# Kernel optimization log

Hardware: AMD Instinct MI355X
Metric: run time of the kernel (lower is better)

Reference implementation:

```python
import jax, jax.numpy as jnp
import numpy as np

B, D_IN, N, K, L, D_OUT = 64, 1024, 50000, 32, 3, 256


def setup_inputs() -> dict:
    key = jax.random.key(0)
    k = jax.random.split(key, 7)
    x = jax.random.normal(k[0], (B, D_IN), dtype=jnp.float32)
    W0 = jax.random.normal(k[1], (N, D_IN), dtype=jnp.float32) * 0.02
    b0 = jax.random.normal(k[2], (N,), dtype=jnp.float32) * 0.02
    Wv = jax.random.normal(k[3], (L, N, K), dtype=jnp.float32) * 0.1
    Wout = jax.random.normal(k[4], (D_OUT, N), dtype=jnp.float32) * 0.02
    bout = jax.random.normal(k[5], (D_OUT,), dtype=jnp.float32) * 0.02
    src = jax.random.randint(k[6], (L, N, K), 0, N, dtype=jnp.int64)
    return {"x": x, "W0": W0, "b0": b0, "Wv": Wv, "Wout": Wout, "bout": bout, "src": src}


def reference(x, W0, b0, Wv, Wout, bout, src):
    # layer 0: dense input->sources, relu, transpose -> [N, B]
    h = jax.nn.relu(x @ W0.T + b0).T

    # each hidden layer: per-vertex gather of K source activations + 1xK matmul + relu
    def step(h_prev, layer):
        w, s = layer                      # w: [N, K], s: [N, K]
        gathered = h_prev[s]              # [N, K, B] irregular gather
        h_new = jax.nn.relu(jnp.einsum('nk,nkb->nb', w, gathered))
        return h_new, None

    h, _ = jax.lax.scan(step, h, (Wv, src))

    # last layer -> output Linear (the module's _linear_dummy)
    return h.T @ Wout.T + bout            # [B, D_OUT]
```

## Files before the change

kernel.cpp:

```cpp
#include <hip/hip_runtime.h>

#define NV 50000
#define NVP 50176
#define BDIM 64
#define DIN 1024
#define KFAN 32
#define DOUT 256
#define KSTEPS (DIN / 32)
#define OPC_CHUNK 128
#define OPC_NCH (NVP / OPC_CHUNK)

typedef short bf16x8 __attribute__((ext_vector_type(8)));
typedef float f32x4 __attribute__((ext_vector_type(4)));

__device__ __forceinline__ unsigned short bf16_rtn(float f) {
  unsigned u = __float_as_uint(f);
  return (unsigned short)((u + 0x7fffu + ((u >> 16) & 1u)) >> 16);
}
__device__ __forceinline__ float bf16_to_f(unsigned short v) {
  return __uint_as_float(((unsigned)v) << 16);
}
__device__ __forceinline__ void gload_lds16(const float* g, float* l) {
  __builtin_amdgcn_global_load_lds(
      (const __attribute__((address_space(1))) void*)g,
      (__attribute__((address_space(3))) void*)l, 16, 0, 0);
}

__global__ __launch_bounds__(256) void pack_x(const float* __restrict__ x,
                                              uint4* __restrict__ xpk) {
  int tid = blockIdx.x * 256 + threadIdx.x;
  int ks = tid >> 8;
  int g = (tid >> 6) & 3;
  int l = tid & 63;
  int b = g * 16 + (l & 15);
  int k0 = ks * 32 + (l >> 4) * 8;
  unsigned hi[8], lo[8];
#pragma unroll
  for (int j = 0; j < 8; ++j) {
    float f = x[b * DIN + k0 + j];
    unsigned u = __float_as_uint(f);
    hi[j] = u >> 16;
    float fh = __uint_as_float(u & 0xffff0000u);
    lo[j] = bf16_rtn(f - fh);
  }
  uint4 vh, vl;
  vh.x = hi[0] | (hi[1] << 16); vh.y = hi[2] | (hi[3] << 16);
  vh.z = hi[4] | (hi[5] << 16); vh.w = hi[6] | (hi[7] << 16);
  vl.x = lo[0] | (lo[1] << 16); vl.y = lo[2] | (lo[3] << 16);
  vl.z = lo[4] | (lo[5] << 16); vl.w = lo[6] | (lo[7] << 16);
  xpk[(ks * 4 + g) * 128 + l] = vh;
  xpk[(ks * 4 + g) * 128 + 64 + l] = vl;
}

__global__ __launch_bounds__(256) void layer0_mfma(
    const float* __restrict__ W0, const float* __restrict__ b0,
    const uint4* __restrict__ xpk, unsigned short* __restrict__ h)
{
  __shared__ float wlds[2][64 * 32];
  const int t = threadIdx.x;
  const int lane = t & 63;
  const int w = t >> 6;
  const int rq = lane >> 4;
  const int rr = lane & 15;
  const int n0 = blockIdx.x * 64;

  int s_row[2], s_srcg[2];
#pragma unroll
  for (int p = 0; p < 2; ++p) {
    int flat = p * 256 + t;
    s_row[p] = flat >> 3;
    s_srcg[p] = (flat & 7) ^ (s_row[p] & 7);
  }
  int rowg0 = n0 + s_row[0]; if (rowg0 > NV - 1) rowg0 = NV - 1;
  int rowg1 = n0 + s_row[1]; if (rowg1 > NV - 1) rowg1 = NV - 1;
  const float* sp0 = W0 + (size_t)rowg0 * DIN + s_srcg[0] * 4;
  const float* sp1 = W0 + (size_t)rowg1 * DIN + s_srcg[1] * 4;

  const int myrow = w * 16 + rr;
  const int sw = (myrow & 7) << 4;
  const int off0 = (myrow * 128 + ((rq * 32) ^ sw)) >> 2;
  const int off1 = (myrow * 128 + ((rq * 32 + 16) ^ sw)) >> 2;

  f32x4 acc[4];
#pragma unroll
  for (int g = 0; g < 4; ++g) acc[g] = (f32x4){0.f, 0.f, 0.f, 0.f};

  gload_lds16(sp0, &wlds[0][(0 * 256 + t) * 4]);
  gload_lds16(sp1, &wlds[0][(1 * 256 + t) * 4]);
  __syncthreads();

  for (int ks = 0; ks < KSTEPS; ++ks) {
    const int cur = ks & 1;
    if (ks + 1 < KSTEPS) {
      const int ko = (ks + 1) * 32;
      gload_lds16(sp0 + ko, &wlds[cur ^ 1][(0 * 256 + t) * 4]);
      gload_lds16(sp1 + ko, &wlds[cur ^ 1][(1 * 256 + t) * 4]);
    }
    const int xb = ks * 512;
    uint4 xc[4][2];
#pragma unroll
    for (int g = 0; g < 4; ++g) {
      xc[g][0] = xpk[xb + g * 128 + lane];
      xc[g][1] = xpk[xb + g * 128 + 64 + lane];
    }
    const float* wb = &wlds[cur][0];
    float4 wv0 = *(const float4*)(wb + off0);
    float4 wv1 = *(const float4*)(wb + off1);
    bf16x8 whi, wlo;
    {
      float wf[8] = {wv0.x, wv0.y, wv0.z, wv0.w, wv1.x, wv1.y, wv1.z, wv1.w};
#pragma unroll
      for (int e = 0; e < 8; ++e) {
        unsigned u = __float_as_uint(wf[e]);
        whi[e] = (short)(u >> 16);
        float l = wf[e] - __uint_as_float(u & 0xffff0000u);
        wlo[e] = (short)bf16_rtn(l);
      }
    }
#pragma unroll
    for (int g = 0; g < 4; ++g) {
      bf16x8 xh = __builtin_bit_cast(bf16x8, xc[g][0]);
      bf16x8 xl = __builtin_bit_cast(bf16x8, xc[g][1]);
      acc[g] = __builtin_amdgcn_mfma_f32_16x16x32_bf16(whi, xh, acc[g], 0, 0, 0);
      acc[g] = __builtin_amdgcn_mfma_f32_16x16x32_bf16(wlo, xh, acc[g], 0, 0, 0);
      acc[g] = __builtin_amdgcn_mfma_f32_16x16x32_bf16(whi, xl, acc[g], 0, 0, 0);
    }
    __syncthreads();
  }

#pragma unroll
  for (int r = 0; r < 4; ++r) {
    int n = n0 + w * 16 + rq * 4 + r;
    if (n < NV) {
      float bias = b0[n];
#pragma unroll
      for (int g = 0; g < 4; ++g) {
        float v = fmaxf(acc[g][r] + bias, 0.f);
        h[(size_t)n * BDIM + g * 16 + rr] = bf16_rtn(v);
      }
    }
  }
}

__global__ __launch_bounds__(256) void sparse_layer(
    const unsigned short* __restrict__ hin, const float* __restrict__ wv,
    const int* __restrict__ src, unsigned short* __restrict__ hout)
{
  const int lane = threadIdx.x & 63;
  int n = blockIdx.x * 4 + (threadIdx.x >> 6);
  n = __builtin_amdgcn_readfirstlane(n);
  const float* wrow = wv + (size_t)n * KFAN;
  const int* srow = src + (size_t)n * KFAN;
  float acc = 0.f;
#pragma unroll
  for (int k = 0; k < KFAN; ++k) {
    int s = srow[k];
    float w = wrow[k];
    acc = fmaf(w, bf16_to_f(hin[(size_t)s * BDIM + lane]), acc);
  }
  hout[(size_t)n * BDIM + lane] = bf16_rtn(fmaxf(acc, 0.f));
}

__global__ __launch_bounds__(256) void transpose_h(
    const unsigned short* __restrict__ h, unsigned short* __restrict__ hT)
{
  const int lane = threadIdx.x & 63;
  const int wv = threadIdx.x >> 6;
  const int n0 = (blockIdx.x * 4 + wv) * 8;
  unsigned short v[8];
#pragma unroll
  for (int i = 0; i < 8; ++i) {
    int n = n0 + i;
    v[i] = (n < NV) ? h[(size_t)n * BDIM + lane] : (unsigned short)0;
  }
  uint4 o;
  o.x = v[0] | ((unsigned)v[1] << 16);
  o.y = v[2] | ((unsigned)v[3] << 16);
  o.z = v[4] | ((unsigned)v[5] << 16);
  o.w = v[6] | ((unsigned)v[7] << 16);
  *(uint4*)(hT + (size_t)lane * NVP + n0) = o;
}

__global__ __launch_bounds__(64) void out_partial_mfma(
    const unsigned short* __restrict__ hT, const float* __restrict__ Wout,
    float* __restrict__ part)
{
  const int lane = threadIdx.x;
  const int rq = lane >> 4;
  const int rr = lane & 15;
  const int dtile = blockIdx.x;
  const int chunk = blockIdx.y;

  f32x4 acc[4][4];
#pragma unroll
  for (int f = 0; f < 4; ++f)
#pragma unroll
    for (int g = 0; g < 4; ++g) acc[f][g] = (f32x4){0.f, 0.f, 0.f, 0.f};

#pragma unroll
  for (int ks = 0; ks < OPC_CHUNK / 32; ++ks) {
    const int n0 = chunk * OPC_CHUNK + ks * 32 + rq * 8;
    bf16x8 hb[4];
#pragma unroll
    for (int g = 0; g < 4; ++g)
      hb[g] = *(const bf16x8*)(hT + (size_t)(g * 16 + rr) * NVP + n0);
    int nb = n0 > (NV - 8) ? (NV - 8) : n0;
#pragma unroll
    for (int f = 0; f < 4; ++f) {
      const float* wp = Wout + (size_t)(dtile * 64 + f * 16 + rr) * NV + nb;
      float4 a0 = *(const float4*)(wp);
      float4 a1 = *(const float4*)(wp + 4);
      float wf[8] = {a0.x, a0.y, a0.z, a0.w, a1.x, a1.y, a1.z, a1.w};
      bf16x8 whi, wlo;
#pragma unroll
      for (int e = 0; e < 8; ++e) {
        unsigned u = __float_as_uint(wf[e]);
        whi[e] = (short)(u >> 16);
        float l = wf[e] - __uint_as_float(u & 0xffff0000u);
        wlo[e] = (short)bf16_rtn(l);
      }
#pragma unroll
      for (int g = 0; g < 4; ++g) {
        acc[f][g] = __builtin_amdgcn_mfma_f32_16x16x32_bf16(whi, hb[g], acc[f][g], 0, 0, 0);
        acc[f][g] = __builtin_amdgcn_mfma_f32_16x16x32_bf16(wlo, hb[g], acc[f][g], 0, 0, 0);
      }
    }
  }
  float* pbase = part + ((size_t)dtile * OPC_NCH + chunk) * 4096;
#pragma unroll
  for (int f = 0; f < 4; ++f)
#pragma unroll
    for (int g = 0; g < 4; ++g)
#pragma unroll
      for (int r = 0; r < 4; ++r)
        pbase[(f * 16 + rq * 4 + r) * 64 + g * 16 + rr] = acc[f][g][r];
}

__global__ __launch_bounds__(256) void out_reduce(
    const float* __restrict__ part, const float* __restrict__ bout,
    float* __restrict__ out)
{
  int tid = blockIdx.x * 256 + threadIdx.x;
  int b = tid & 63;
  int d = tid >> 6;
  int dtile = d >> 6;
  int dd = d & 63;
  float s = bout[d];
  for (int c = 0; c < OPC_NCH; ++c)
    s += part[((size_t)dtile * OPC_NCH + c) * 4096 + dd * 64 + b];
  out[(size_t)b * DOUT + d] = s;
}

extern "C" void kernel_launch(void* const* d_in, const int* in_sizes, int n_in,
                              void* d_out, int out_size, void* d_ws, size_t ws_size,
                              hipStream_t stream)
{
  const float* x    = (const float*)d_in[0];
  const float* W0   = (const float*)d_in[1];
  const float* b0   = (const float*)d_in[2];
  const float* Wv   = (const float*)d_in[3];
  const float* Wout = (const float*)d_in[4];
  const float* bout = (const float*)d_in[5];
  const int*   src  = (const int*)d_in[6];
  float* out = (float*)d_out;

  char* ws = (char*)d_ws;
  const size_t hbf = (size_t)NV * BDIM * 2;
  const size_t hTb = (size_t)NVP * BDIM * 2;
  unsigned short* hb0 = (unsigned short*)ws;
  unsigned short* hb1 = (unsigned short*)(ws + hbf);
  unsigned short* hT  = (unsigned short*)(ws + 2 * hbf);
  uint4* xpk  = (uint4*)(ws + 2 * hbf + hTb);
  float* part = (float*)(ws + 2 * hbf + hTb);

  pack_x<<<32, 256, 0, stream>>>(x, xpk);
  layer0_mfma<<<(NV + 63) / 64, 256, 0, stream>>>(W0, b0, xpk, hb0);

  const size_t lstride = (size_t)NV * KFAN;
  sparse_layer<<<NV / 4, 256, 0, stream>>>(hb0, Wv, src, hb1);
  sparse_layer<<<NV / 4, 256, 0, stream>>>(hb1, Wv + lstride, src + lstride, hb0);
  sparse_layer<<<NV / 4, 256, 0, stream>>>(hb0, Wv + 2 * lstride, src + 2 * lstride, hb1);

  transpose_h<<<NVP / 32, 256, 0, stream>>>(hb1, hT);
  out_partial_mfma<<<dim3(4, OPC_NCH), 64, 0, stream>>>(hT, Wout, part);
  out_reduce<<<(BDIM * DOUT) / 256, 256, 0, stream>>>(part, bout, out);
}
```

Before: 202.4 us.

## Stage packed x through LDS with async loads and replicate it per XCD

Result: faster. 185.8 us (median of 2 runs) (-8.2%).

```diff
diff --git a/kernel.cpp b/kernel.cpp
--- a/kernel.cpp
+++ b/kernel.cpp
@@ -7,6 +7,7 @@
 #define KFAN 32
 #define DOUT 256
 #define KSTEPS (DIN / 32)
+#define XPK_N (KSTEPS * 512)
 #define OPC_CHUNK 128
 #define OPC_NCH (NVP / OPC_CHUNK)
 
@@ -20,14 +21,14 @@
 __device__ __forceinline__ float bf16_to_f(unsigned short v) {
   return __uint_as_float(((unsigned)v) << 16);
 }
-__device__ __forceinline__ void gload_lds16(const float* g, float* l) {
+__device__ __forceinline__ void gload_lds16(const void* g, void* l) {
   __builtin_amdgcn_global_load_lds(
       (const __attribute__((address_space(1))) void*)g,
       (__attribute__((address_space(3))) void*)l, 16, 0, 0);
 }
 
 __global__ __launch_bounds__(256) void pack_x(const float* __restrict__ x,
-                                              uint4* __restrict__ xpk) {
+                                              uint4* __restrict__ xpk8) {
   int tid = blockIdx.x * 256 + threadIdx.x;
   int ks = tid >> 8;
   int g = (tid >> 6) & 3;
@@ -48,21 +49,27 @@
   vh.z = hi[4] | (hi[5] << 16); vh.w = hi[6] | (hi[7] << 16);
   vl.x = lo[0] | (lo[1] << 16); vl.y = lo[2] | (lo[3] << 16);
   vl.z = lo[4] | (lo[5] << 16); vl.w = lo[6] | (lo[7] << 16);
-  xpk[(ks * 4 + g) * 128 + l] = vh;
-  xpk[(ks * 4 + g) * 128 + 64 + l] = vl;
+  int idx = (ks * 4 + g) * 128 + l;
+#pragma unroll
+  for (int c = 0; c < 8; ++c) {
+    xpk8[(size_t)c * XPK_N + idx] = vh;
+    xpk8[(size_t)c * XPK_N + idx + 64] = vl;
+  }
 }
 
 __global__ __launch_bounds__(256) void layer0_mfma(
     const float* __restrict__ W0, const float* __restrict__ b0,
-    const uint4* __restrict__ xpk, unsigned short* __restrict__ h)
+    const uint4* __restrict__ xpk8, unsigned short* __restrict__ h)
 {
   __shared__ float wlds[2][64 * 32];
+  __shared__ uint4 xlds[2][512];
   const int t = threadIdx.x;
   const int lane = t & 63;
   const int w = t >> 6;
   const int rq = lane >> 4;
   const int rr = lane & 15;
   const int n0 = blockIdx.x * 64;
+  const uint4* xsrc = xpk8 + (size_t)(blockIdx.x & 7) * XPK_N;
 
   int s_row[2], s_srcg[2];
 #pragma unroll
@@ -87,6 +94,8 @@
 
   gload_lds16(sp0, &wlds[0][(0 * 256 + t) * 4]);
   gload_lds16(sp1, &wlds[0][(1 * 256 + t) * 4]);
+  gload_lds16(xsrc + (0 * 256 + t), &xlds[0][0 * 256 + t]);
+  gload_lds16(xsrc + (1 * 256 + t), &xlds[0][1 * 256 + t]);
   __syncthreads();
 
   for (int ks = 0; ks < KSTEPS; ++ks) {
@@ -95,13 +104,15 @@
       const int ko = (ks + 1) * 32;
       gload_lds16(sp0 + ko, &wlds[cur ^ 1][(0 * 256 + t) * 4]);
       gload_lds16(sp1 + ko, &wlds[cur ^ 1][(1 * 256 + t) * 4]);
-    }
-    const int xb = ks * 512;
+      const uint4* xs = xsrc + (ks + 1) * 512;
+      gload_lds16(xs + (0 * 256 + t), &xlds[cur ^ 1][0 * 256 + t]);
+      gload_lds16(xs + (1 * 256 + t), &xlds[cur ^ 1][1 * 256 + t]);
+    }
     uint4 xc[4][2];
 #pragma unroll
     for (int g = 0; g < 4; ++g) {
-      xc[g][0] = xpk[xb + g * 128 + lane];
-      xc[g][1] = xpk[xb + g * 128 + 64 + lane];
+      xc[g][0] = xlds[cur][g * 128 + lane];
+      xc[g][1] = xlds[cur][g * 128 + 64 + lane];
     }
     const float* wb = &wlds[cur][0];
     float4 wv0 = *(const float4*)(wb + off0);
@@ -267,14 +278,15 @@
   char* ws = (char*)d_ws;
   const size_t hbf = (size_t)NV * BDIM * 2;
   const size_t hTb = (size_t)NVP * BDIM * 2;
+  const size_t xpkb = (size_t)8 * XPK_N * 16;
   unsigned short* hb0 = (unsigned short*)ws;
   unsigned short* hb1 = (unsigned short*)(ws + hbf);
   unsigned short* hT  = (unsigned short*)(ws + 2 * hbf);
-  uint4* xpk  = (uint4*)(ws + 2 * hbf + hTb);
-  float* part = (float*)(ws + 2 * hbf + hTb);
-
-  pack_x<<<32, 256, 0, stream>>>(x, xpk);
-  layer0_mfma<<<(NV + 63) / 64, 256, 0, stream>>>(W0, b0, xpk, hb0);
+  uint4* xpk8 = (uint4*)(ws + 2 * hbf + hTb);
+  float* part = (float*)(ws + 2 * hbf + hTb + xpkb);
+
+  pack_x<<<32, 256, 0, stream>>>(x, xpk8);
+  layer0_mfma<<<(NV + 63) / 64, 256, 0, stream>>>(W0, b0, xpk8, hb0);
 
   const size_t lstride = (size_t)NV * KFAN;
   sparse_layer<<<NV / 4, 256, 0, stream>>>(hb0, Wv, src, hb1);
```
